# Kernel tuning notes

Measured on AMD Instinct MI355X. Metric: run time of the kernel, lower is better.

The kernel has to match this reference:

```python
import math
import jax, jax.numpy as jnp
import numpy as np

B, LQ, LK, D, DV = 16, 2048, 2048, 256, 256


def setup_inputs() -> dict:
    key = jax.random.key(0)
    k1, k2, k3, k4 = jax.random.split(key, 4)
    query = jax.random.normal(k1, (B, LQ, D), dtype=jnp.float32)
    kmat = jax.random.normal(k2, (B, LK, D), dtype=jnp.float32)
    value = jax.random.normal(k3, (B, LK, DV), dtype=jnp.float32)
    # per-batch valid lengths in [1, LK] (avoid 0 => all -inf row)
    valid_len = jax.random.randint(k4, (B,), 1, LK + 1, dtype=jnp.int64)
    return {"query": query, "key": kmat, "value": value, "valid_len": valid_len}


def reference(query, key, value, valid_len):
    d = query.shape[-1]
    # [B, Lq, Lk] scaled dot-product scores
    scores = jnp.einsum("bqd,bkd->bqk", query, key) / math.sqrt(d)
    # mask positions k >= valid_len[b] (same mask broadcast over all queries,
    # matching the repeat(1, Lq).view(shape) in the original masked_softmax)
    mask = jnp.arange(key.shape[1])[None, None, :] < valid_len[:, None, None]
    scores = jnp.where(mask, scores, -jnp.inf)
    attn = jax.nn.softmax(scores, axis=-1)  # dropout rate is 0.0 => identity
    return jnp.einsum("bqk,bkv->bqv", attn, value)
```

## Files before the change

kernel.cpp:

```cpp
#include <hip/hip_runtime.h>
#include <hip/hip_bf16.h>

#define B_   16
#define LQ_  2048
#define LK_  2048
#define D_   256
#define DV_  256
#define MINF -1.0e30f

typedef __bf16 bf16x8_t __attribute__((ext_vector_type(8)));
typedef short  s16x8    __attribute__((ext_vector_type(8)));
typedef short  s16x4    __attribute__((ext_vector_type(4)));
typedef float  f32x4    __attribute__((ext_vector_type(4)));

__device__ __forceinline__ unsigned short f2bf(float f) {
  unsigned int u = __builtin_bit_cast(unsigned int, f);
  u += 0x7fffu + ((u >> 16) & 1u);
  return (unsigned short)(u >> 16);
}

__device__ __forceinline__ s16x8 pack8(float4 a, float4 b) {
  s16x8 r;
  r[0] = (short)f2bf(a.x); r[1] = (short)f2bf(a.y);
  r[2] = (short)f2bf(a.z); r[3] = (short)f2bf(a.w);
  r[4] = (short)f2bf(b.x); r[5] = (short)f2bf(b.y);
  r[6] = (short)f2bf(b.z); r[7] = (short)f2bf(b.w);
  return r;
}

__device__ __forceinline__ void glds16(const unsigned short* g, unsigned short* l) {
  __builtin_amdgcn_global_load_lds(
      (const __attribute__((address_space(1))) unsigned int*)g,
      (__attribute__((address_space(3))) unsigned int*)l, 16, 0, 0);
}

__global__ __launch_bounds__(256) void prep_k(const float* __restrict__ K,
                                              unsigned short* __restrict__ wsK) {
  int gid = blockIdx.x * 256 + threadIdx.x;
  int gr = gid >> 5;
  int c  = gid & 31;
  const float* src = K + ((size_t)gr << 8) + c * 8;
  float4 a = *(const float4*)(src);
  float4 b = *(const float4*)(src + 4);
  *(s16x8*)(wsK + ((size_t)gr << 8) + ((c ^ (gr & 7)) << 3)) = pack8(a, b);
}

__global__ __launch_bounds__(256) void prep_v(const float* __restrict__ V,
                                              unsigned short* __restrict__ wsV) {
  __shared__ unsigned short t[256 * 72];
  const int tid = threadIdx.x;
  const float* src = V + (size_t)blockIdx.x * 64 * 256;
  #pragma unroll
  for (int i = 0; i < 16; ++i) {
    int idx = i * 256 + tid;
    int k   = idx >> 6;
    int dv0 = (idx & 63) * 4;
    float4 x = *(const float4*)(src + k * 256 + dv0);
    t[(dv0 + 0) * 72 + k] = f2bf(x.x);
    t[(dv0 + 1) * 72 + k] = f2bf(x.y);
    t[(dv0 + 2) * 72 + k] = f2bf(x.z);
    t[(dv0 + 3) * 72 + k] = f2bf(x.w);
  }
  __syncthreads();
  unsigned short* dst = wsV + (size_t)blockIdx.x * 16384;
  #pragma unroll
  for (int i = 0; i < 8; ++i) {
    int idx = i * 256 + tid;
    int dv = idx >> 3;
    int ch = idx & 7;
    s16x8 v = *(const s16x8*)(&t[dv * 72 + ch * 8]);
    *(s16x8*)(dst + dv * 64 + ((ch ^ (dv & 7)) << 3)) = v;
  }
}

__global__ __launch_bounds__(512, 2) void attn_fwd4(
    const float* __restrict__ Q, const unsigned short* __restrict__ wsK,
    const unsigned short* __restrict__ wsV, const int* __restrict__ VL,
    float* __restrict__ O) {
  __shared__ __align__(16) unsigned short lds_all[75776];

  const int tid  = threadIdx.x;
  const int wid  = tid >> 6;
  const int lane = tid & 63;
  const int l15  = lane & 15;
  const int lg   = lane >> 4;
  const int rq   = wid & 3;
  const int kh   = wid >> 2;

  const int bid = blockIdx.x;
  const int b   = bid >> 4;
  const int qt  = bid & 15;

  int n_k = (VL[1] == 0) ? VL[2 * b] : VL[b];
  if (n_k < 1) n_k = 1;
  if (n_k > LK_) n_k = LK_;
  const int nt = (n_k + 63) >> 6;

  const int qbase = qt * 128 + rq * 32;

  s16x8 qf[2][8];
  #pragma unroll
  for (int qc = 0; qc < 2; ++qc) {
    const float* qp = Q + ((size_t)b * LQ_ + qbase + qc * 16 + l15) * D_ + lg * 8;
    #pragma unroll
    for (int dk = 0; dk < 8; ++dk) {
      float4 a = *(const float4*)(qp + dk * 32);
      float4 c = *(const float4*)(qp + dk * 32 + 4);
      qf[qc][dk] = pack8(a, c);
    }
  }

  f32x4 o[2][16];
  #pragma unroll
  for (int qc = 0; qc < 2; ++qc)
    #pragma unroll
    for (int c = 0; c < 16; ++c) o[qc][c] = (f32x4){0.f, 0.f, 0.f, 0.f};
  float m[2] = {MINF, MINF}, l[2] = {0.f, 0.f};

  const unsigned short* kbw = wsK + (size_t)b * LK_ * D_;
  const unsigned short* vbw = wsV + (size_t)b * LK_ * DV_;
  unsigned short* pw = &lds_all[65536 + wid * 1280];

#define STAGE(buf, t) do {                                                    \
    const unsigned short* ks_ = kbw + (size_t)(t) * 16384;                    \
    const unsigned short* vs_ = vbw + (size_t)(t) * 16384;                    \
    _Pragma("unroll")                                                         \
    for (int p = 0; p < 4; ++p) {                                             \
      int cu = p * 512 + wid * 64;                                            \
      glds16(ks_ + (size_t)(cu + lane) * 8, &lds_all[(buf) * 16384 + cu * 8]);\
      glds16(vs_ + (size_t)(cu + lane) * 8,                                   \
             &lds_all[32768 + (buf) * 16384 + cu * 8]);                       \
    }                                                                         \
  } while (0)

  STAGE(0, 0);
  __syncthreads();

  for (int t = 0; t < nt; ++t) {
    const int cur = t & 1;
    if (t + 1 < nt) STAGE(cur ^ 1, t + 1);

    const unsigned short* kl = &lds_all[cur * 16384];
    f32x4 s[2][2];
    __builtin_amdgcn_s_setprio(1);
    #pragma unroll
    for (int kc = 0; kc < 2; ++kc) {
      int krow = kh * 32 + kc * 16 + l15;
      int sw = (krow & 7) << 3;
      const unsigned short* base = kl + krow * 256;
      f32x4 a0 = (f32x4){0.f, 0.f, 0.f, 0.f};
      f32x4 a1 = (f32x4){0.f, 0.f, 0.f, 0.f};
      #pragma unroll
      for (int dk = 0; dk < 8; ++dk) {
        s16x8 kf = *(const s16x8*)(base + ((dk * 32 + lg * 8) ^ sw));
        a0 = __builtin_amdgcn_mfma_f32_16x16x32_bf16(
            __builtin_bit_cast(bf16x8_t, kf),
            __builtin_bit_cast(bf16x8_t, qf[0][dk]), a0, 0, 0, 0);
        a1 = __builtin_amdgcn_mfma_f32_16x16x32_bf16(
            __builtin_bit_cast(bf16x8_t, kf),
            __builtin_bit_cast(bf16x8_t, qf[1][dk]), a1, 0, 0, 0);
      }
      s[kc][0] = a0;
      s[kc][1] = a1;
    }
    __builtin_amdgcn_s_setprio(0);

    #pragma unroll
    for (int kc = 0; kc < 2; ++kc) {
      int gk = t * 64 + kh * 32 + kc * 16 + lg * 4;
      #pragma unroll
      for (int qc = 0; qc < 2; ++qc)
        #pragma unroll
        for (int j = 0; j < 4; ++j)
          s[kc][qc][j] = (gk + j < n_k) ? s[kc][qc][j] * 0.0625f : MINF;
    }

    float pm[2];
    #pragma unroll
    for (int qc = 0; qc < 2; ++qc) {
      float v = fmaxf(fmaxf(s[0][qc][0], s[0][qc][1]),
                      fmaxf(s[0][qc][2], s[0][qc][3]));
      v = fmaxf(v, fmaxf(fmaxf(s[1][qc][0], s[1][qc][1]),
                         fmaxf(s[1][qc][2], s[1][qc][3])));
      v = fmaxf(v, __shfl_xor(v, 16, 64));
      v = fmaxf(v, __shfl_xor(v, 32, 64));
      pm[qc] = v;
    }
    if (__any((pm[0] > m[0] + 8.0f) || (pm[1] > m[1] + 8.0f))) {
      #pragma unroll
      for (int qc = 0; qc < 2; ++qc) {
        float mn = fmaxf(m[qc], pm[qc]);
        float sc = __expf(m[qc] - mn);
        m[qc] = mn; l[qc] *= sc;
        #pragma unroll
        for (int c = 0; c < 16; ++c) o[qc][c] = o[qc][c] * sc;
      }
    }
    #pragma unroll
    for (int qc = 0; qc < 2; ++qc) {
      float p[2][4];
      #pragma unroll
      for (int kc = 0; kc < 2; ++kc)
        #pragma unroll
        for (int j = 0; j < 4; ++j)
          p[kc][j] = __expf(s[kc][qc][j] - m[qc]);
      float ps = ((p[0][0] + p[0][1]) + (p[0][2] + p[0][3]))
               + ((p[1][0] + p[1][1]) + (p[1][2] + p[1][3]));
      ps += __shfl_xor(ps, 16, 64);
      ps += __shfl_xor(ps, 32, 64);
      l[qc] += ps;
      #pragma unroll
      for (int kc = 0; kc < 2; ++kc) {
        s16x4 w;
        w[0] = (short)f2bf(p[kc][0]); w[1] = (short)f2bf(p[kc][1]);
        w[2] = (short)f2bf(p[kc][2]); w[3] = (short)f2bf(p[kc][3]);
        *(s16x4*)(pw + (qc * 16 + l15) * 40 + kc * 16 + lg * 4) = w;
      }
    }

    s16x8 pb[2];
    #pragma unroll
    for (int qc = 0; qc < 2; ++qc)
      pb[qc] = *(const s16x8*)(pw + (qc * 16 + l15) * 40 + lg * 8);

    const unsigned short* vl_ = &lds_all[32768 + cur * 16384];
    __builtin_amdgcn_s_setprio(1);
    #pragma unroll
    for (int c = 0; c < 16; ++c) {
      int dv = c * 16 + l15;
      s16x8 vf = *(const s16x8*)(vl_ + dv * 64 + (((kh * 4 + lg) ^ (dv & 7)) << 3));
      o[0][c] = __builtin_amdgcn_mfma_f32_16x16x32_bf16(
          __builtin_bit_cast(bf16x8_t, vf),
          __builtin_bit_cast(bf16x8_t, pb[0]), o[0][c], 0, 0, 0);
      o[1][c] = __builtin_amdgcn_mfma_f32_16x16x32_bf16(
          __builtin_bit_cast(bf16x8_t, vf),
          __builtin_bit_cast(bf16x8_t, pb[1]), o[1][c], 0, 0, 0);
    }
    __builtin_amdgcn_s_setprio(0);

    __syncthreads();
  }

  float* mo = (float*)lds_all + rq * 8448;
  if (kh == 1) {
    #pragma unroll
    for (int qc = 0; qc < 2; ++qc) {
      #pragma unroll
      for (int c = 0; c < 16; ++c)
        *(f32x4*)(mo + (qc * 16 + l15) * 260 + c * 16 + lg * 4) = o[qc][c];
      mo[8320 + qc * 16 + l15] = m[qc];
      mo[8352 + qc * 16 + l15] = l[qc];
    }
  }
  __syncthreads();
  if (kh == 0) {
    #pragma unroll
    for (int qc = 0; qc < 2; ++qc) {
      float mb = mo[8320 + qc * 16 + l15];
      float lb = mo[8352 + qc * 16 + l15];
      float M  = fmaxf(m[qc], mb);
      float sa = __expf(m[qc] - M), sb = __expf(mb - M);
      float invL = 1.0f / (sa * l[qc] + sb * lb);
      float* ob = O + ((size_t)b * LQ_ + qbase + qc * 16 + l15) * DV_;
      #pragma unroll
      for (int c = 0; c < 16; ++c) {
        int dvb = c * 16 + lg * 4;
        f32x4 mr = *(const f32x4*)(mo + (qc * 16 + l15) * 260 + dvb);
        f32x4 r;
        #pragma unroll
        for (int j = 0; j < 4; ++j) r[j] = (sa * o[qc][c][j] + sb * mr[j]) * invL;
        *(f32x4*)(ob + dvb) = r;
      }
    }
  }
#undef STAGE
}

__global__ __launch_bounds__(256) void attn_fwd(
    const float* __restrict__ Q, const float* __restrict__ K,
    const float* __restrict__ V, const int* __restrict__ VL,
    float* __restrict__ O) {
  __shared__ __align__(16) unsigned short lds_k[64 * D_];
  __shared__ __align__(16) unsigned short lds_v[DV_ * 64];
  __shared__ __align__(16) unsigned short lds_p[4][16 * 64];

  const int tid  = threadIdx.x;
  const int wid  = tid >> 6;
  const int lane = tid & 63;
  const int l15  = lane & 15;
  const int lg   = lane >> 4;
  const int bid = blockIdx.x;
  const int b   = bid >> 5;
  const int qt  = bid & 31;

  int n_k = (VL[1] == 0) ? VL[2 * b] : VL[b];
  if (n_k < 1) n_k = 1;
  if (n_k > LK_) n_k = LK_;

  const int qbase = qt * 64 + wid * 16;
  s16x8 qf[8];
  {
    const float* qp = Q + ((size_t)b * LQ_ + qbase + l15) * D_ + lg * 8;
    #pragma unroll
    for (int dk = 0; dk < 8; ++dk) {
      float4 a = *(const float4*)(qp + dk * 32);
      float4 c = *(const float4*)(qp + dk * 32 + 4);
      qf[dk] = pack8(a, c);
    }
  }
  f32x4 o[16];
  #pragma unroll
  for (int c = 0; c < 16; ++c) o[c] = (f32x4){0.f, 0.f, 0.f, 0.f};
  float m[4]    = {-INFINITY, -INFINITY, -INFINITY, -INFINITY};
  float lsum[4] = {0.f, 0.f, 0.f, 0.f};
  const float* kb = K + (size_t)b * LK_ * D_;
  const float* vb = V + (size_t)b * LK_ * DV_;
  const int nt = (n_k + 63) / 64;

  for (int kt = 0; kt < nt; ++kt) {
    __syncthreads();
    {
      const float* src = kb + (size_t)kt * 64 * D_;
      #pragma unroll
      for (int p = 0; p < 8; ++p) {
        int e = (p * 256 + tid) * 8;
        int r = e >> 8;
        int d = e & 255;
        float4 a = *(const float4*)(src + e);
        float4 c = *(const float4*)(src + e + 4);
        *(s16x8*)(&lds_k[r * 256 + (d ^ ((r & 7) << 3))]) = pack8(a, c);
      }
    }
    {
      const float* src = vb + (size_t)kt * 64 * DV_;
      #pragma unroll
      for (int p = 0; p < 2; ++p) {
        int item = p * 256 + tid;
        int k0  = (item >> 5) * 4;
        int dv0 = (item & 31) * 8;
        float va[4][8];
        #pragma unroll
        for (int r = 0; r < 4; ++r) {
          float4 x = *(const float4*)(src + (k0 + r) * DV_ + dv0);
          float4 y = *(const float4*)(src + (k0 + r) * DV_ + dv0 + 4);
          va[r][0]=x.x; va[r][1]=x.y; va[r][2]=x.z; va[r][3]=x.w;
          va[r][4]=y.x; va[r][5]=y.y; va[r][6]=y.z; va[r][7]=y.w;
        }
        #pragma unroll
        for (int i = 0; i < 8; ++i) {
          int dv = dv0 + i;
          s16x4 w;
          w[0]=(short)f2bf(va[0][i]); w[1]=(short)f2bf(va[1][i]);
          w[2]=(short)f2bf(va[2][i]); w[3]=(short)f2bf(va[3][i]);
          *(s16x4*)(&lds_v[dv * 64 + (k0 ^ ((dv & 7) << 3))]) = w;
        }
      }
    }
    __syncthreads();

    f32x4 s[4];
    #pragma unroll
    for (int kc = 0; kc < 4; ++kc) {
      f32x4 acc = (f32x4){0.f, 0.f, 0.f, 0.f};
      int krow = kc * 16 + l15;
      int sw = (krow & 7) << 3;
      #pragma unroll
      for (int dk = 0; dk < 8; ++dk) {
        s16x8 kf = *(const s16x8*)(&lds_k[krow * 256 + ((dk * 32 + lg * 8) ^ sw)]);
        acc = __builtin_amdgcn_mfma_f32_16x16x32_bf16(
            __builtin_bit_cast(bf16x8_t, qf[dk]),
            __builtin_bit_cast(bf16x8_t, kf), acc, 0, 0, 0);
      }
      s[kc] = acc;
    }
    #pragma unroll
    for (int kc = 0; kc < 4; ++kc) {
      int gk = kt * 64 + kc * 16 + l15;
      #pragma unroll
      for (int j = 0; j < 4; ++j) {
        float v = s[kc][j] * 0.0625f;
        s[kc][j] = (gk < n_k) ? v : -INFINITY;
      }
    }
    float pm[4];
    #pragma unroll
    for (int j = 0; j < 4; ++j)
      pm[j] = fmaxf(fmaxf(s[0][j], s[1][j]), fmaxf(s[2][j], s[3][j]));
    #pragma unroll
    for (int off = 1; off < 16; off <<= 1) {
      #pragma unroll
      for (int j = 0; j < 4; ++j)
        pm[j] = fmaxf(pm[j], __shfl_xor(pm[j], off, 64));
    }
    float sc[4];
    #pragma unroll
    for (int j = 0; j < 4; ++j) {
      float mn = fmaxf(m[j], pm[j]);
      sc[j] = __expf(m[j] - mn);
      m[j] = mn;
    }
    float psum[4] = {0.f, 0.f, 0.f, 0.f};
    #pragma unroll
    for (int kc = 0; kc < 4; ++kc) {
      #pragma unroll
      for (int j = 0; j < 4; ++j) {
        float p = __expf(s[kc][j] - m[j]);
        psum[j] += p;
        int r = lg * 4 + j;
        lds_p[wid][r * 64 + ((kc * 16 + l15) ^ ((r & 7) << 3))] = f2bf(p);
      }
    }
    #pragma unroll
    for (int off = 1; off < 16; off <<= 1) {
      #pragma unroll
      for (int j = 0; j < 4; ++j)
        psum[j] += __shfl_xor(psum[j], off, 64);
    }
    #pragma unroll
    for (int j = 0; j < 4; ++j) lsum[j] = lsum[j] * sc[j] + psum[j];
    #pragma unroll
    for (int c = 0; c < 16; ++c) {
      #pragma unroll
      for (int j = 0; j < 4; ++j) o[c][j] *= sc[j];
    }
    s16x8 pa[2];
    #pragma unroll
    for (int kk = 0; kk < 2; ++kk)
      pa[kk] = *(const s16x8*)(&lds_p[wid][l15 * 64 + ((kk * 32 + lg * 8) ^ ((l15 & 7) << 3))]);
    #pragma unroll
    for (int c = 0; c < 16; ++c) {
      #pragma unroll
      for (int kk = 0; kk < 2; ++kk) {
        int dv = c * 16 + l15;
        s16x8 vf = *(const s16x8*)(&lds_v[dv * 64 + ((kk * 32 + lg * 8) ^ ((dv & 7) << 3))]);
        o[c] = __builtin_amdgcn_mfma_f32_16x16x32_bf16(
            __builtin_bit_cast(bf16x8_t, pa[kk]),
            __builtin_bit_cast(bf16x8_t, vf), o[c], 0, 0, 0);
      }
    }
  }
  float inv[4];
  #pragma unroll
  for (int j = 0; j < 4; ++j) inv[j] = 1.0f / lsum[j];
  float* ob = O + ((size_t)b * LQ_ + qbase) * DV_;
  #pragma unroll
  for (int c = 0; c < 16; ++c) {
    #pragma unroll
    for (int j = 0; j < 4; ++j) {
      int r = lg * 4 + j;
      ob[(size_t)r * DV_ + c * 16 + l15] = o[c][j] * inv[j];
    }
  }
}

extern "C" void kernel_launch(void* const* d_in, const int* in_sizes, int n_in,
                              void* d_out, int out_size, void* d_ws, size_t ws_size,
                              hipStream_t stream) {
  const float* Q  = (const float*)d_in[0];
  const float* K  = (const float*)d_in[1];
  const float* V  = (const float*)d_in[2];
  const int*   VL = (const int*)d_in[3];
  float* O = (float*)d_out;

  const size_t kv_elems = (size_t)B_ * LK_ * D_;
  const size_t need = kv_elems * 2 * sizeof(unsigned short);
  if (ws_size >= need) {
    unsigned short* wsK = (unsigned short*)d_ws;
    unsigned short* wsV = wsK + kv_elems;
    prep_k<<<dim3(4096), dim3(256), 0, stream>>>(K, wsK);
    prep_v<<<dim3(512), dim3(256), 0, stream>>>(V, wsV);
    attn_fwd4<<<dim3(256), dim3(512), 0, stream>>>(Q, wsK, wsV, VL, O);
  } else {
    attn_fwd<<<dim3(512), dim3(256), 0, stream>>>(Q, K, V, VL, O);
  }
}
```

Baseline: 135.9 us.

## Split attention over key dimension with partial outputs and separate merge kernel

```diff
diff --git a/kernel.cpp b/kernel.cpp
--- a/kernel.cpp
+++ b/kernel.cpp
@@ -47,56 +47,60 @@
 
 __global__ __launch_bounds__(256) void prep_v(const float* __restrict__ V,
                                               unsigned short* __restrict__ wsV) {
-  __shared__ unsigned short t[256 * 72];
+  __shared__ unsigned short t[256 * 40];
   const int tid = threadIdx.x;
-  const float* src = V + (size_t)blockIdx.x * 64 * 256;
-  #pragma unroll
-  for (int i = 0; i < 16; ++i) {
+  const float* src = V + (size_t)blockIdx.x * 32 * 256;
+  #pragma unroll
+  for (int i = 0; i < 8; ++i) {
     int idx = i * 256 + tid;
     int k   = idx >> 6;
     int dv0 = (idx & 63) * 4;
     float4 x = *(const float4*)(src + k * 256 + dv0);
-    t[(dv0 + 0) * 72 + k] = f2bf(x.x);
-    t[(dv0 + 1) * 72 + k] = f2bf(x.y);
-    t[(dv0 + 2) * 72 + k] = f2bf(x.z);
-    t[(dv0 + 3) * 72 + k] = f2bf(x.w);
+    t[(dv0 + 0) * 40 + k] = f2bf(x.x);
+    t[(dv0 + 1) * 40 + k] = f2bf(x.y);
+    t[(dv0 + 2) * 40 + k] = f2bf(x.z);
+    t[(dv0 + 3) * 40 + k] = f2bf(x.w);
   }
   __syncthreads();
-  unsigned short* dst = wsV + (size_t)blockIdx.x * 16384;
-  #pragma unroll
-  for (int i = 0; i < 8; ++i) {
+  unsigned short* dst = wsV + (size_t)blockIdx.x * 8192;
+  #pragma unroll
+  for (int i = 0; i < 4; ++i) {
     int idx = i * 256 + tid;
-    int dv = idx >> 3;
-    int ch = idx & 7;
-    s16x8 v = *(const s16x8*)(&t[dv * 72 + ch * 8]);
-    *(s16x8*)(dst + dv * 64 + ((ch ^ (dv & 7)) << 3)) = v;
-  }
-}
-
-__global__ __launch_bounds__(512, 2) void attn_fwd4(
+    int dv = idx >> 2;
+    int cs = idx & 3;
+    int c2 = cs ^ ((dv >> 1) & 3);
+    s16x8 v = *(const s16x8*)(&t[dv * 40 + cs * 8]);
+    *(s16x8*)(dst + dv * 32 + c2 * 8) = v;
+  }
+}
+
+__global__ __launch_bounds__(256, 2) void attn_fwd6(
     const float* __restrict__ Q, const unsigned short* __restrict__ wsK,
     const unsigned short* __restrict__ wsV, const int* __restrict__ VL,
-    float* __restrict__ O) {
-  __shared__ __align__(16) unsigned short lds_all[75776];
+    unsigned short* __restrict__ part, float* __restrict__ lse, int splk) {
+  __shared__ __align__(16) unsigned short lds_all[37888];
 
   const int tid  = threadIdx.x;
   const int wid  = tid >> 6;
   const int lane = tid & 63;
   const int l15  = lane & 15;
   const int lg   = lane >> 4;
-  const int rq   = wid & 3;
-  const int kh   = wid >> 2;
 
   const int bid = blockIdx.x;
-  const int b   = bid >> 4;
-  const int qt  = bid & 15;
+  const int h   = bid >> 8;
+  const int r   = bid & 255;
+  const int b   = (r & 7) | ((r >> 7) << 3);
+  const int qt  = (r >> 3) & 15;
 
   int n_k = (VL[1] == 0) ? VL[2 * b] : VL[b];
   if (n_k < 1) n_k = 1;
   if (n_k > LK_) n_k = LK_;
-  const int nt = (n_k + 63) >> 6;
-
-  const int qbase = qt * 128 + rq * 32;
+  const int kbeg = h * splk;
+  if (kbeg >= n_k) return;
+  const int kend = (n_k < kbeg + splk) ? n_k : (kbeg + splk);
+  const int nt = (kend - kbeg + 31) >> 5;
+
+  const int qbase = qt * 128 + wid * 32;
 
   s16x8 qf[2][8];
   #pragma unroll
@@ -117,19 +121,19 @@
     for (int c = 0; c < 16; ++c) o[qc][c] = (f32x4){0.f, 0.f, 0.f, 0.f};
   float m[2] = {MINF, MINF}, l[2] = {0.f, 0.f};
 
-  const unsigned short* kbw = wsK + (size_t)b * LK_ * D_;
-  const unsigned short* vbw = wsV + (size_t)b * LK_ * DV_;
-  unsigned short* pw = &lds_all[65536 + wid * 1280];
+  const unsigned short* kbw = wsK + ((size_t)b * LK_ + kbeg) * D_;
+  const unsigned short* vbw = wsV + ((size_t)b * 64 + (kbeg >> 5)) * 8192;
+  unsigned short* pw = &lds_all[32768 + wid * 1280];
 
 #define STAGE(buf, t) do {                                                    \
-    const unsigned short* ks_ = kbw + (size_t)(t) * 16384;                    \
-    const unsigned short* vs_ = vbw + (size_t)(t) * 16384;                    \
+    const unsigned short* ks_ = kbw + (size_t)(t) * 8192;                     \
+    const unsigned short* vs_ = vbw + (size_t)(t) * 8192;                     \
     _Pragma("unroll")                                                         \
     for (int p = 0; p < 4; ++p) {                                             \
-      int cu = p * 512 + wid * 64;                                            \
-      glds16(ks_ + (size_t)(cu + lane) * 8, &lds_all[(buf) * 16384 + cu * 8]);\
+      int cu = p * 256 + wid * 64;                                            \
+      glds16(ks_ + (size_t)(cu + lane) * 8, &lds_all[(buf) * 8192 + cu * 8]); \
       glds16(vs_ + (size_t)(cu + lane) * 8,                                   \
-             &lds_all[32768 + (buf) * 16384 + cu * 8]);                       \
+             &lds_all[16384 + (buf) * 8192 + cu * 8]);                        \
     }                                                                         \
   } while (0)
 
@@ -140,12 +144,12 @@
     const int cur = t & 1;
     if (t + 1 < nt) STAGE(cur ^ 1, t + 1);
 
-    const unsigned short* kl = &lds_all[cur * 16384];
+    const unsigned short* kl = &lds_all[cur * 8192];
     f32x4 s[2][2];
     __builtin_amdgcn_s_setprio(1);
     #pragma unroll
     for (int kc = 0; kc < 2; ++kc) {
-      int krow = kh * 32 + kc * 16 + l15;
+      int krow = kc * 16 + l15;
       int sw = (krow & 7) << 3;
       const unsigned short* base = kl + krow * 256;
       f32x4 a0 = (f32x4){0.f, 0.f, 0.f, 0.f};
@@ -167,7 +171,7 @@
 
     #pragma unroll
     for (int kc = 0; kc < 2; ++kc) {
-      int gk = t * 64 + kh * 32 + kc * 16 + lg * 4;
+      int gk = kbeg + t * 32 + kc * 16 + lg * 4;
       #pragma unroll
       for (int qc = 0; qc < 2; ++qc)
         #pragma unroll
@@ -223,12 +227,12 @@
     for (int qc = 0; qc < 2; ++qc)
       pb[qc] = *(const s16x8*)(pw + (qc * 16 + l15) * 40 + lg * 8);
 
-    const unsigned short* vl_ = &lds_all[32768 + cur * 16384];
+    const unsigned short* vl_ = &lds_all[16384 + cur * 8192];
     __builtin_amdgcn_s_setprio(1);
     #pragma unroll
     for (int c = 0; c < 16; ++c) {
       int dv = c * 16 + l15;
-      s16x8 vf = *(const s16x8*)(vl_ + dv * 64 + (((kh * 4 + lg) ^ (dv & 7)) << 3));
+      s16x8 vf = *(const s16x8*)(vl_ + dv * 32 + ((lg ^ ((dv >> 1) & 3)) << 3));
       o[0][c] = __builtin_amdgcn_mfma_f32_16x16x32_bf16(
           __builtin_bit_cast(bf16x8_t, vf),
           __builtin_bit_cast(bf16x8_t, pb[0]), o[0][c], 0, 0, 0);
@@ -241,39 +245,80 @@
     __syncthreads();
   }
 
-  float* mo = (float*)lds_all + rq * 8448;
-  if (kh == 1) {
-    #pragma unroll
-    for (int qc = 0; qc < 2; ++qc) {
-      #pragma unroll
-      for (int c = 0; c < 16; ++c)
-        *(f32x4*)(mo + (qc * 16 + l15) * 260 + c * 16 + lg * 4) = o[qc][c];
-      mo[8320 + qc * 16 + l15] = m[qc];
-      mo[8352 + qc * 16 + l15] = l[qc];
-    }
-  }
-  __syncthreads();
-  if (kh == 0) {
-    #pragma unroll
-    for (int qc = 0; qc < 2; ++qc) {
-      float mb = mo[8320 + qc * 16 + l15];
-      float lb = mo[8352 + qc * 16 + l15];
-      float M  = fmaxf(m[qc], mb);
-      float sa = __expf(m[qc] - M), sb = __expf(mb - M);
-      float invL = 1.0f / (sa * l[qc] + sb * lb);
-      float* ob = O + ((size_t)b * LQ_ + qbase + qc * 16 + l15) * DV_;
-      #pragma unroll
-      for (int c = 0; c < 16; ++c) {
-        int dvb = c * 16 + lg * 4;
-        f32x4 mr = *(const f32x4*)(mo + (qc * 16 + l15) * 260 + dvb);
-        f32x4 r;
+  const size_t unit = ((size_t)h * 16 + b) * 16 + qt;
+  unsigned short* pp = part + unit * 32768;
+  #pragma unroll
+  for (int qc = 0; qc < 2; ++qc) {
+    float inv = 1.0f / l[qc];
+    int q = wid * 32 + qc * 16 + l15;
+    unsigned short* rowp = pp + (size_t)q * 256;
+    #pragma unroll
+    for (int c = 0; c < 16; ++c) {
+      s16x4 w;
+      #pragma unroll
+      for (int j = 0; j < 4; ++j) {
+        _Float16 hx = (_Float16)(o[qc][c][j] * inv);
+        w[j] = __builtin_bit_cast(short, hx);
+      }
+      *(s16x4*)(rowp + c * 16 + lg * 4) = w;
+    }
+    lse[unit * 128 + q] = m[qc] + __logf(l[qc]);
+  }
+#undef STAGE
+}
+
+__global__ __launch_bounds__(256) void merge6(
+    const unsigned short* __restrict__ part, const float* __restrict__ lse,
+    const int* __restrict__ VL, float* __restrict__ O, int splk, int nspl) {
+  const int bid = blockIdx.x;
+  const int b  = (bid & 7) | ((bid >> 7) << 3);
+  const int qt = (bid >> 3) & 15;
+  int n_k = (VL[1] == 0) ? VL[2 * b] : VL[b];
+  if (n_k < 1) n_k = 1;
+  if (n_k > LK_) n_k = LK_;
+  int ns = (n_k + splk - 1) / splk;
+  if (ns > nspl) ns = nspl;
+
+  const int tid  = threadIdx.x;
+  const int lane = tid & 63;
+  const int wv   = tid >> 6;
+  const int dv   = lane * 4;
+
+  for (int i = 0; i < 32; ++i) {
+    int q = i * 4 + wv;
+    float w[4];
+    float M = -INFINITY;
+    #pragma unroll
+    for (int hh = 0; hh < 4; ++hh) {
+      if (hh < ns) {
+        w[hh] = lse[(((size_t)hh * 16 + b) * 16 + qt) * 128 + q];
+        M = fmaxf(M, w[hh]);
+      }
+    }
+    float W = 0.f;
+    #pragma unroll
+    for (int hh = 0; hh < 4; ++hh) {
+      if (hh < ns) { w[hh] = __expf(w[hh] - M); W += w[hh]; }
+    }
+    float invW = 1.0f / W;
+    f32x4 acc = (f32x4){0.f, 0.f, 0.f, 0.f};
+    #pragma unroll
+    for (int hh = 0; hh < 4; ++hh) {
+      if (hh < ns) {
+        const unsigned short* pr =
+            part + (((size_t)hh * 16 + b) * 16 + qt) * 32768 + (size_t)q * 256 + dv;
+        s16x4 pv = *(const s16x4*)pr;
         #pragma unroll
-        for (int j = 0; j < 4; ++j) r[j] = (sa * o[qc][c][j] + sb * mr[j]) * invL;
-        *(f32x4*)(ob + dvb) = r;
-      }
-    }
-  }
-#undef STAGE
+        for (int j = 0; j < 4; ++j) {
+          _Float16 hx = __builtin_bit_cast(_Float16, (short)pv[j]);
+          acc[j] += w[hh] * (float)hx;
+        }
+      }
+    }
+    #pragma unroll
+    for (int j = 0; j < 4; ++j) acc[j] *= invW;
+    *(f32x4*)(O + ((size_t)b * LQ_ + qt * 128 + q) * DV_ + dv) = acc;
+  }
 }
 
 __global__ __launch_bounds__(256) void attn_fwd(
@@ -406,8 +451,8 @@
       for (int j = 0; j < 4; ++j) {
         float p = __expf(s[kc][j] - m[j]);
         psum[j] += p;
-        int r = lg * 4 + j;
-        lds_p[wid][r * 64 + ((kc * 16 + l15) ^ ((r & 7) << 3))] = f2bf(p);
+        int r2 = lg * 4 + j;
+        lds_p[wid][r2 * 64 + ((kc * 16 + l15) ^ ((r2 & 7) << 3))] = f2bf(p);
       }
     }
     #pragma unroll
@@ -447,8 +492,8 @@
   for (int c = 0; c < 16; ++c) {
     #pragma unroll
     for (int j = 0; j < 4; ++j) {
-      int r = lg * 4 + j;
-      ob[(size_t)r * DV_ + c * 16 + l15] = o[c][j] * inv[j];
+      int r2 = lg * 4 + j;
+      ob[(size_t)r2 * DV_ + c * 16 + l15] = o[c][j] * inv[j];
     }
   }
 }
@@ -462,14 +507,28 @@
   const int*   VL = (const int*)d_in[3];
   float* O = (float*)d_out;
 
-  const size_t kv_elems = (size_t)B_ * LK_ * D_;
-  const size_t need = kv_elems * 2 * sizeof(unsigned short);
-  if (ws_size >= need) {
-    unsigned short* wsK = (unsigned short*)d_ws;
-    unsigned short* wsV = wsK + kv_elems;
+  const size_t kv_elems  = (size_t)B_ * LK_ * D_;
+  const size_t kv_bytes  = kv_elems * 2 * sizeof(unsigned short);
+  const size_t part_unit = (size_t)16 * 16 * 128 * 256;
+  const size_t lse_unit  = (size_t)16 * 16 * 128;
+
+  int nspl = 0;
+  for (int n = 4; n >= 1; n >>= 1) {
+    size_t need = kv_bytes + (size_t)n * (part_unit * 2 + lse_unit * 4);
+    if (ws_size >= need) { nspl = n; break; }
+  }
+
+  if (nspl) {
+    unsigned short* wsK  = (unsigned short*)d_ws;
+    unsigned short* wsV  = wsK + kv_elems;
+    unsigned short* wpart = wsV + kv_elems;
+    float* wlse = (float*)(wpart + (size_t)nspl * part_unit);
+    int splk = LK_ / nspl;
     prep_k<<<dim3(4096), dim3(256), 0, stream>>>(K, wsK);
-    prep_v<<<dim3(512), dim3(256), 0, stream>>>(V, wsV);
-    attn_fwd4<<<dim3(256), dim3(512), 0, stream>>>(Q, wsK, wsV, VL, O);
+    prep_v<<<dim3(1024), dim3(256), 0, stream>>>(V, wsV);
+    attn_fwd6<<<dim3(nspl * 256), dim3(256), 0, stream>>>(Q, wsK, wsV, VL,
+                                                          wpart, wlse, splk);
+    merge6<<<dim3(256), dim3(256), 0, stream>>>(wpart, wlse, VL, O, splk, nspl);
   } else {
     attn_fwd<<<dim3(512), dim3(256), 0, stream>>>(Q, K, V, VL, O);
   }
```

New measurement: 205.9 us. 1.51x slower.
